# Optimization experiments

Measured on AMD Instinct MI355X. Metric: run time of the kernel, lower is better.

The kernel has to match this reference:

```python
import jax, jax.numpy as jnp
import numpy as np

ALPHA = 0.2  # LeakyReLU negative slope

def setup_inputs() -> dict:
    key = jax.random.key(0)
    k1, k2, k3 = jax.random.split(key, 3)
    N, H, Wd, T, V = 4, 16, 16, 32, 32
    h = jax.random.normal(k1, (N, H, Wd, T, V), dtype=jnp.float32)
    W = jax.random.normal(k2, (T, T), dtype=jnp.float32) * 0.1   # (in_features, out_features), xavier-like scale
    a = jax.random.normal(k3, (2 * H * Wd, 1), dtype=jnp.float32) * 0.05
    B_adj = jnp.zeros((V, V), dtype=jnp.float32)
    return {"h": h, "W": W, "a": a, "B_adj": B_adj}


def reference(h, W, a, B_adj):
    N, H, Wd, T, V = h.shape
    HW = H * Wd
    # (N,H,W,T,V) -> (N,V,H,W,T)
    hv = jnp.transpose(h, (0, 4, 1, 2, 3))
    Wh = jnp.matmul(hv, W)  # (N,V,H,W,T), out_features == T

    # pairwise attentional input: repeat_interleave / tile, concat along the W axis,
    # then the (faithful) mixed reshape (H,2W,T) -> (T,2HW)
    Wh_i = jnp.repeat(Wh, V, axis=1)            # (N,V*V,H,W,T), node i in chunks
    Wh_j = jnp.tile(Wh, (1, V, 1, 1, 1))        # (N,V*V,H,W,T), node j alternating
    a_input = jnp.concatenate([Wh_i, Wh_j], axis=-2)          # (N,V*V,H,2W,T)
    a_input = a_input.reshape(N, V, V, T, 2 * HW)

    e = jnp.matmul(a_input, a)[..., 0]          # (N,V,V,T)
    e = jnp.where(e > 0, e, ALPHA * e)          # LeakyReLU
    attention = jax.nn.softmax(e, axis=-1)      # softmax over T

    # graph-Laplacian normalized adjacency
    adj = (B_adj + 1e-6) + jnp.eye(V, dtype=B_adj.dtype)
    adj = (adj - jnp.min(adj)) / (jnp.max(adj) - jnp.min(adj))
    d_isqrt = 1.0 / jnp.sqrt(jnp.sum(adj, axis=1))
    adj_norm = adj * d_isqrt[:, None] * d_isqrt[None, :]  # D^-1/2 A D^-1/2

    # aggregation: h_prime[n,c,t,i] = sum_j Wh[n,j,c,t] * attention[n,i,j,t]
    Wh_flat = Wh.reshape(N, V, HW, T)
    h_prime = jnp.einsum('njct,nijt->ncti', Wh_flat, attention)  # (N,HW,T,V)

    h_prime = jnp.matmul(h_prime, adj_norm)     # (N,HW,T,V)
    h_prime = h_prime.reshape(N, H, Wd, T, V)
    return jax.nn.elu(h_prime)
```

## Files before the change

### kernel.cpp

```cpp
#include <hip/hip_runtime.h>
#include <math.h>


#define ALPHA 0.2f

__global__ __launch_bounds__(256) void k_adjnorm(const float* __restrict__ B,
                                                 float* __restrict__ adjn_g) {
    __shared__ float nrm[1024];
    __shared__ float red[64];
    __shared__ float dis[32];
    __shared__ float mnmx[2];
    int tid = threadIdx.x;
    float vals[4];
    float lmn = 1e30f, lmx = -1e30f;
    for (int k = 0; k < 4; ++k) {
        int e = tid + 256 * k;
        float x = B[e] + 1e-6f + (((e >> 5) == (e & 31)) ? 1.0f : 0.0f);
        vals[k] = x;
        lmn = fminf(lmn, x);
        lmx = fmaxf(lmx, x);
    }
    for (int m = 1; m < 64; m <<= 1) {
        lmn = fminf(lmn, __shfl_xor(lmn, m));
        lmx = fmaxf(lmx, __shfl_xor(lmx, m));
    }
    int wid = tid >> 6;
    if ((tid & 63) == 0) { red[wid] = lmn; red[32 + wid] = lmx; }
    __syncthreads();
    if (tid == 0) {
        float mn = fminf(fminf(red[0], red[1]), fminf(red[2], red[3]));
        float mx = fmaxf(fmaxf(red[32], red[33]), fmaxf(red[34], red[35]));
        mnmx[0] = mn; mnmx[1] = mx;
    }
    __syncthreads();
    float mn = mnmx[0];
    float inv = 1.0f / (mnmx[1] - mn);
    for (int k = 0; k < 4; ++k) {
        int e = tid + 256 * k;
        nrm[e] = (vals[k] - mn) * inv;
    }
    __syncthreads();
    if (tid < 32) {
        float rs = 0.f;
        for (int i = 0; i < 32; ++i) rs += nrm[tid * 32 + i];
        dis[tid] = 1.0f / sqrtf(rs);
    }
    __syncthreads();
    for (int k = 0; k < 4; ++k) {
        int e = tid + 256 * k;
        adjn_g[e] = nrm[e] * dis[e >> 5] * dis[e & 31];
    }
}

__global__ __launch_bounds__(256) void k_wh(const float* __restrict__ h,
                                            const float* __restrict__ Wm,
                                            float* __restrict__ Wh,
                                            float* __restrict__ WhT) {
    __shared__ float ht[1024];
    __shared__ float Wl[1024];
    int tid = threadIdx.x;
    int bid = blockIdx.x;
    int n = bid >> 8, c = bid & 255;
    const float4* hsrc = (const float4*)(h + ((size_t)(n * 256 + c)) * 1024);
    ((float4*)ht)[tid] = hsrc[tid];
    ((float4*)Wl)[tid] = ((const float4*)Wm)[tid];
    __syncthreads();
    int tp = tid & 31, v0 = tid >> 5;
    for (int p = 0; p < 4; ++p) {
        int v = v0 + 8 * p;
        float acc = 0.f;
#pragma unroll
        for (int t = 0; t < 32; ++t)
            acc = fmaf(ht[t * 32 + v], Wl[t * 32 + tp], acc);
        Wh[(((size_t)(n * 32 + v)) * 256 + c) * 32 + tp] = acc;
        WhT[(((size_t)(n * 32 + tp)) * 256 + c) * 32 + v] = acc;
    }
}

__global__ __launch_bounds__(256) void k_softstats(const float* __restrict__ Wh,
                                                   const float* __restrict__ a,
                                                   float* __restrict__ u_g,
                                                   float* __restrict__ mx_g,
                                                   float* __restrict__ E_g) {
    __shared__ float su[16];
    int tid = threadIdx.x;
    int nv = blockIdx.x;
    int m = tid >> 4, l = tid & 15;
    const float* base = Wh + (size_t)nv * 8192 + m * 512;
    float acc = 0.f;
    for (int k = 0; k < 32; ++k) {
        int e = k * 16 + l;
        acc = fmaf(base[e], a[e], acc);
    }
    for (int msk = 1; msk < 16; msk <<= 1) acc += __shfl_xor(acc, msk, 16);
    float u = acc > 0.f ? acc : ALPHA * acc;
    if (l == 0) su[m] = u;
    __syncthreads();
    if (tid < 16) {
        float uu = su[tid];
        float mxv = uu;
        for (int msk = 1; msk < 16; msk <<= 1) mxv = fmaxf(mxv, __shfl_xor(mxv, msk, 16));
        float ex = expf(uu - mxv);
        float es = ex;
        for (int msk = 1; msk < 16; msk <<= 1) es += __shfl_xor(es, msk, 16);
        u_g[nv * 16 + tid] = uu;
        if (tid == 0) { mx_g[nv] = mxv; E_g[nv] = es; }
    }
}

__global__ __launch_bounds__(256) void k_out(const float* __restrict__ WhT,
                                             const float* __restrict__ u_g,
                                             const float* __restrict__ mx_g,
                                             const float* __restrict__ E_g,
                                             const float* __restrict__ adjn_g,
                                             float* __restrict__ out) {
    __shared__ float wht[8192];
    __shared__ float A[1024];
    __shared__ float gt[1024];
    __shared__ float adjn[1024];
    __shared__ float un[32], mxl[32], El[32];
    int tid = threadIdx.x;
    int bid = blockIdx.x;
    int n = bid >> 5, tp = bid & 31;
    int m = tp >> 1, odd = tp & 1;
    const float4* src = (const float4*)(WhT + ((size_t)(n * 32 + tp)) * 8192);
#pragma unroll
    for (int k = 0; k < 8; ++k)
        ((float4*)wht)[tid + 256 * k] = src[tid + 256 * k];
    ((float4*)adjn)[tid] = ((const float4*)adjn_g)[tid];
    if (tid < 32) {
        un[tid]  = u_g[(n * 32 + tid) * 16 + m];
        mxl[tid] = mx_g[n * 32 + tid];
        El[tid]  = E_g[n * 32 + tid];
    }
    __syncthreads();
    {
        int j = tid & 31, v0 = tid >> 5;
        for (int p = 0; p < 4; ++p) {
            int v = v0 + 8 * p;
            float mv = mxl[v], mj = mxl[j];
            float M = fmaxf(mv, mj);
            float Z = El[v] * expf(mv - M) + El[j] * expf(mj - M);
            float num = odd ? expf(un[j] - M) : expf(un[v] - M);
            A[v * 32 + j] = num / Z;
        }
    }
    __syncthreads();
    {
        int i = tid & 31, j0 = tid >> 5;
        for (int p = 0; p < 4; ++p) {
            int j = j0 + 8 * p;
            float acc = 0.f;
#pragma unroll
            for (int v = 0; v < 32; ++v)
                acc = fmaf(adjn[v * 32 + i], A[v * 32 + j], acc);
            gt[j * 32 + i] = acc;
        }
    }
    __syncthreads();
    {
        int i = tid & 31, cg = tid >> 5;
        float greg[32];
#pragma unroll
        for (int j = 0; j < 32; ++j) greg[j] = gt[j * 32 + i];
        for (int k = 0; k < 32; ++k) {
            int c = cg * 32 + k;
            float acc = 0.f;
#pragma unroll
            for (int j8 = 0; j8 < 8; ++j8) {
                float4 w4 = ((float4*)wht)[c * 8 + j8];
                acc = fmaf(greg[4 * j8 + 0], w4.x, acc);
                acc = fmaf(greg[4 * j8 + 1], w4.y, acc);
                acc = fmaf(greg[4 * j8 + 2], w4.z, acc);
                acc = fmaf(greg[4 * j8 + 3], w4.w, acc);
            }
            float o = acc > 0.f ? acc : expm1f(acc);
            out[(((size_t)(n * 256 + c)) * 32 + tp) * 32 + i] = o;
        }
    }
}

extern "C" void kernel_launch(void* const* d_in, const int* in_sizes, int n_in,
                              void* d_out, int out_size, void* d_ws, size_t ws_size,
                              hipStream_t stream) {
    const float* h  = (const float*)d_in[0];
    const float* Wm = (const float*)d_in[1];
    const float* a  = (const float*)d_in[2];
    const float* B  = (const float*)d_in[3];
    float* out = (float*)d_out;
    float* ws  = (float*)d_ws;

    float* Wh   = ws;
    float* WhT  = ws + 1048576;
    float* u_g  = ws + 2097152;
    float* mx_g = u_g + 2048;
    float* E_g  = mx_g + 128;
    float* adjn = E_g + 128;

    k_adjnorm<<<1, 256, 0, stream>>>(B, adjn);
    k_wh<<<1024, 256, 0, stream>>>(h, Wm, Wh, WhT);
    k_softstats<<<128, 256, 0, stream>>>(Wh, a, u_g, mx_g, E_g);
    k_out<<<128, 256, 0, stream>>>(WhT, u_g, mx_g, E_g, adjn, out);
}
```

Baseline: 85.75 us.

## Fuse Wh, score dot-product and adjacency norm into two kernels

Merges the four kernels into two. The first kernel computes Wh, reduces the attention score contribution with shuffles and atomicAdd into a small buffer, and writes only the transposed WhT through a padded shared tile to get coalesced stores. The second kernel recomputes the adjacency normalisation and the softmax statistics per block before doing the aggregation. This removes the separate Wh write/read, two kernel launches, and the single-block adjnorm kernel. In exchange it adds a memset, float atomics whose summation order is nondeterministic, and redundant per-block adjacency work.

```diff
diff --git a/kernel.cpp b/kernel.cpp
--- a/kernel.cpp
+++ b/kernel.cpp
@@ -4,156 +4,141 @@
 
 #define ALPHA 0.2f
 
-__global__ __launch_bounds__(256) void k_adjnorm(const float* __restrict__ B,
-                                                 float* __restrict__ adjn_g) {
-    __shared__ float nrm[1024];
-    __shared__ float red[64];
-    __shared__ float dis[32];
-    __shared__ float mnmx[2];
-    int tid = threadIdx.x;
-    float vals[4];
-    float lmn = 1e30f, lmx = -1e30f;
-    for (int k = 0; k < 4; ++k) {
-        int e = tid + 256 * k;
-        float x = B[e] + 1e-6f + (((e >> 5) == (e & 31)) ? 1.0f : 0.0f);
-        vals[k] = x;
-        lmn = fminf(lmn, x);
-        lmx = fmaxf(lmx, x);
+__global__ __launch_bounds__(256) void k_whs(const float* __restrict__ h,
+                                             const float* __restrict__ Wm,
+                                             const float* __restrict__ a,
+                                             float* __restrict__ WhT,
+                                             float* __restrict__ s_g) {
+    __shared__ float ht[1024];
+    __shared__ float Wl[1024];
+    __shared__ float S[32 * 33];
+    int tid = threadIdx.x, bid = blockIdx.x;
+    int n = bid >> 8, c = bid & 255;
+    int w = c & 15, m = c >> 4;
+    ((float4*)ht)[tid] = ((const float4*)(h + ((size_t)(n * 256 + c)) * 1024))[tid];
+    ((float4*)Wl)[tid] = ((const float4*)Wm)[tid];
+    __syncthreads();
+    int tp = tid & 31, v0 = tid >> 5;
+    float acc[4] = {0.f, 0.f, 0.f, 0.f};
+#pragma unroll
+    for (int t = 0; t < 32; ++t) {
+        float wl = Wl[t * 32 + tp];
+#pragma unroll
+        for (int p = 0; p < 4; ++p)
+            acc[p] = fmaf(ht[t * 32 + v0 + 8 * p], wl, acc[p]);
     }
-    for (int m = 1; m < 64; m <<= 1) {
-        lmn = fminf(lmn, __shfl_xor(lmn, m));
-        lmx = fmaxf(lmx, __shfl_xor(lmx, m));
-    }
-    int wid = tid >> 6;
-    if ((tid & 63) == 0) { red[wid] = lmn; red[32 + wid] = lmx; }
-    __syncthreads();
-    if (tid == 0) {
-        float mn = fminf(fminf(red[0], red[1]), fminf(red[2], red[3]));
-        float mx = fmaxf(fmaxf(red[32], red[33]), fmaxf(red[34], red[35]));
-        mnmx[0] = mn; mnmx[1] = mx;
+    float av = a[w * 32 + tp];
+#pragma unroll
+    for (int p = 0; p < 4; ++p) {
+        S[tp * 33 + v0 + 8 * p] = acc[p];
+        float contrib = acc[p] * av;
+#pragma unroll
+        for (int msk = 1; msk <= 16; msk <<= 1) contrib += __shfl_xor(contrib, msk);
+        if (tp == 0) atomicAdd(&s_g[(n * 32 + v0 + 8 * p) * 16 + m], contrib);
     }
     __syncthreads();
-    float mn = mnmx[0];
-    float inv = 1.0f / (mnmx[1] - mn);
-    for (int k = 0; k < 4; ++k) {
-        int e = tid + 256 * k;
-        nrm[e] = (vals[k] - mn) * inv;
-    }
-    __syncthreads();
-    if (tid < 32) {
-        float rs = 0.f;
-        for (int i = 0; i < 32; ++i) rs += nrm[tid * 32 + i];
-        dis[tid] = 1.0f / sqrtf(rs);
-    }
-    __syncthreads();
-    for (int k = 0; k < 4; ++k) {
-        int e = tid + 256 * k;
-        adjn_g[e] = nrm[e] * dis[e >> 5] * dis[e & 31];
+#pragma unroll
+    for (int p = 0; p < 4; ++p) {
+        int r = (tid >> 5) + 8 * p, vc = tid & 31;
+        WhT[(((size_t)(n * 32 + r)) * 256 + c) * 32 + vc] = S[r * 33 + vc];
     }
 }
 
-__global__ __launch_bounds__(256) void k_wh(const float* __restrict__ h,
-                                            const float* __restrict__ Wm,
-                                            float* __restrict__ Wh,
-                                            float* __restrict__ WhT) {
-    __shared__ float ht[1024];
-    __shared__ float Wl[1024];
-    int tid = threadIdx.x;
-    int bid = blockIdx.x;
-    int n = bid >> 8, c = bid & 255;
-    const float4* hsrc = (const float4*)(h + ((size_t)(n * 256 + c)) * 1024);
-    ((float4*)ht)[tid] = hsrc[tid];
-    ((float4*)Wl)[tid] = ((const float4*)Wm)[tid];
-    __syncthreads();
-    int tp = tid & 31, v0 = tid >> 5;
-    for (int p = 0; p < 4; ++p) {
-        int v = v0 + 8 * p;
-        float acc = 0.f;
-#pragma unroll
-        for (int t = 0; t < 32; ++t)
-            acc = fmaf(ht[t * 32 + v], Wl[t * 32 + tp], acc);
-        Wh[(((size_t)(n * 32 + v)) * 256 + c) * 32 + tp] = acc;
-        WhT[(((size_t)(n * 32 + tp)) * 256 + c) * 32 + v] = acc;
-    }
-}
-
-__global__ __launch_bounds__(256) void k_softstats(const float* __restrict__ Wh,
-                                                   const float* __restrict__ a,
-                                                   float* __restrict__ u_g,
-                                                   float* __restrict__ mx_g,
-                                                   float* __restrict__ E_g) {
-    __shared__ float su[16];
-    int tid = threadIdx.x;
-    int nv = blockIdx.x;
-    int m = tid >> 4, l = tid & 15;
-    const float* base = Wh + (size_t)nv * 8192 + m * 512;
-    float acc = 0.f;
-    for (int k = 0; k < 32; ++k) {
-        int e = k * 16 + l;
-        acc = fmaf(base[e], a[e], acc);
-    }
-    for (int msk = 1; msk < 16; msk <<= 1) acc += __shfl_xor(acc, msk, 16);
-    float u = acc > 0.f ? acc : ALPHA * acc;
-    if (l == 0) su[m] = u;
-    __syncthreads();
-    if (tid < 16) {
-        float uu = su[tid];
-        float mxv = uu;
-        for (int msk = 1; msk < 16; msk <<= 1) mxv = fmaxf(mxv, __shfl_xor(mxv, msk, 16));
-        float ex = expf(uu - mxv);
-        float es = ex;
-        for (int msk = 1; msk < 16; msk <<= 1) es += __shfl_xor(es, msk, 16);
-        u_g[nv * 16 + tid] = uu;
-        if (tid == 0) { mx_g[nv] = mxv; E_g[nv] = es; }
-    }
-}
-
-__global__ __launch_bounds__(256) void k_out(const float* __restrict__ WhT,
-                                             const float* __restrict__ u_g,
-                                             const float* __restrict__ mx_g,
-                                             const float* __restrict__ E_g,
-                                             const float* __restrict__ adjn_g,
-                                             float* __restrict__ out) {
+__global__ __launch_bounds__(256) void k_outf(const float* __restrict__ WhT,
+                                              const float* __restrict__ s_g,
+                                              const float* __restrict__ B,
+                                              float* __restrict__ out) {
     __shared__ float wht[8192];
-    __shared__ float A[1024];
+    __shared__ float adjn[1024];
+    __shared__ float Aat[1024];
     __shared__ float gt[1024];
-    __shared__ float adjn[1024];
-    __shared__ float un[32], mxl[32], El[32];
-    int tid = threadIdx.x;
-    int bid = blockIdx.x;
+    __shared__ float u[512];
+    __shared__ float mxs[32], Es[32], dis[32];
+    __shared__ float red[8];
+    __shared__ float mnmx[2];
+    int tid = threadIdx.x, bid = blockIdx.x;
     int n = bid >> 5, tp = bid & 31;
     int m = tp >> 1, odd = tp & 1;
     const float4* src = (const float4*)(WhT + ((size_t)(n * 32 + tp)) * 8192);
 #pragma unroll
-    for (int k = 0; k < 8; ++k)
-        ((float4*)wht)[tid + 256 * k] = src[tid + 256 * k];
-    ((float4*)adjn)[tid] = ((const float4*)adjn_g)[tid];
+    for (int k = 0; k < 8; ++k) ((float4*)wht)[tid + 256 * k] = src[tid + 256 * k];
+
+    float4 b4 = ((const float4*)B)[tid];
+    float lmn = 1e30f, lmx = -1e30f;
+    const float* b4f = (const float*)&b4;
+#pragma unroll
+    for (int k = 0; k < 4; ++k) {
+        int e = tid * 4 + k;
+        float x = b4f[k] + 1e-6f + (((e >> 5) == (e & 31)) ? 1.0f : 0.0f);
+        lmn = fminf(lmn, x); lmx = fmaxf(lmx, x);
+        adjn[e] = x;
+    }
+    for (int msk = 1; msk < 64; msk <<= 1) {
+        lmn = fminf(lmn, __shfl_xor(lmn, msk));
+        lmx = fmaxf(lmx, __shfl_xor(lmx, msk));
+    }
+    if ((tid & 63) == 0) { red[tid >> 6] = lmn; red[4 + (tid >> 6)] = lmx; }
+
+    {
+        float s0 = s_g[n * 512 + tid];
+        float s1 = s_g[n * 512 + 256 + tid];
+        u[tid] = s0 > 0.f ? s0 : ALPHA * s0;
+        u[tid + 256] = s1 > 0.f ? s1 : ALPHA * s1;
+    }
+    __syncthreads();
+    if (tid == 0) {
+        float mn = fminf(fminf(red[0], red[1]), fminf(red[2], red[3]));
+        float mx = fmaxf(fmaxf(red[4], red[5]), fmaxf(red[6], red[7]));
+        mnmx[0] = mn; mnmx[1] = 1.0f / (mx - mn);
+    }
+    __syncthreads();
+    float mn = mnmx[0], inv = mnmx[1];
     if (tid < 32) {
-        un[tid]  = u_g[(n * 32 + tid) * 16 + m];
-        mxl[tid] = mx_g[n * 32 + tid];
-        El[tid]  = E_g[n * 32 + tid];
+        float rs = 0.f;
+#pragma unroll
+        for (int k = 0; k < 32; ++k) {
+            int i = (k + tid) & 31;
+            rs += (adjn[tid * 32 + i] - mn) * inv;
+        }
+        dis[tid] = rsqrtf(rs);
+    } else if (tid >= 64 && tid < 96) {
+        int v = tid - 64;
+        float mxv = -1e30f;
+#pragma unroll
+        for (int k = 0; k < 16; ++k) mxv = fmaxf(mxv, u[v * 16 + k]);
+        float es = 0.f;
+#pragma unroll
+        for (int k = 0; k < 16; ++k) es += expf(u[v * 16 + k] - mxv);
+        mxs[v] = mxv; Es[v] = es;
     }
     __syncthreads();
     {
-        int j = tid & 31, v0 = tid >> 5;
+        int j = tid & 31, v0g = tid >> 5;
+#pragma unroll
+        for (int k = 0; k < 4; ++k) {
+            int e = tid * 4 + k;
+            adjn[e] = (adjn[e] - mn) * inv * dis[e >> 5] * dis[e & 31];
+        }
+#pragma unroll
         for (int p = 0; p < 4; ++p) {
-            int v = v0 + 8 * p;
-            float mv = mxl[v], mj = mxl[j];
+            int v = v0g + 8 * p;
+            float mv = mxs[v], mj = mxs[j];
             float M = fmaxf(mv, mj);
-            float Z = El[v] * expf(mv - M) + El[j] * expf(mj - M);
-            float num = odd ? expf(un[j] - M) : expf(un[v] - M);
-            A[v * 32 + j] = num / Z;
+            float Z = Es[v] * expf(mv - M) + Es[j] * expf(mj - M);
+            float num = expf((odd ? u[j * 16 + m] : u[v * 16 + m]) - M);
+            Aat[v * 32 + j] = num / Z;
         }
     }
     __syncthreads();
     {
         int i = tid & 31, j0 = tid >> 5;
+#pragma unroll
         for (int p = 0; p < 4; ++p) {
             int j = j0 + 8 * p;
             float acc = 0.f;
 #pragma unroll
             for (int v = 0; v < 32; ++v)
-                acc = fmaf(adjn[v * 32 + i], A[v * 32 + j], acc);
+                acc = fmaf(adjn[v * 32 + i], Aat[v * 32 + j], acc);
             gt[j * 32 + i] = acc;
         }
     }
@@ -190,15 +175,10 @@
     float* out = (float*)d_out;
     float* ws  = (float*)d_ws;
 
-    float* Wh   = ws;
-    float* WhT  = ws + 1048576;
-    float* u_g  = ws + 2097152;
-    float* mx_g = u_g + 2048;
-    float* E_g  = mx_g + 128;
-    float* adjn = E_g + 128;
+    float* WhT = ws;
+    float* s_g = ws + 1048576;
 
-    k_adjnorm<<<1, 256, 0, stream>>>(B, adjn);
-    k_wh<<<1024, 256, 0, stream>>>(h, Wm, Wh, WhT);
-    k_softstats<<<128, 256, 0, stream>>>(Wh, a, u_g, mx_g, E_g);
-    k_out<<<128, 256, 0, stream>>>(WhT, u_g, mx_g, E_g, adjn, out);
+    hipMemsetAsync(s_g, 0, 2048 * sizeof(float), stream);
+    k_whs<<<1024, 256, 0, stream>>>(h, Wm, a, WhT, s_g);
+    k_outf<<<128, 256, 0, stream>>>(WhT, s_g, B, out);
 }
```

Result: slower. 88.31 us (+3.0%).
